# Optimization experiments

Measured on AMD Instinct MI355X. Metric: run time of the kernel, lower is better.

Reference implementation:

```python
import jax, jax.numpy as jnp
import numpy as np


def _gcn_conv(h, src, dst, W, b, n):
    # PyG GCNConv: x @ W, then symmetric-normalized aggregation with self-loops
    deg = jax.ops.segment_sum(jnp.ones(src.shape[0], h.dtype), dst, num_segments=n)
    dinv = jax.lax.rsqrt(jnp.maximum(deg, 1.0))  # deg >= 1 because self-loops are included
    norm = dinv[src] * dinv[dst]                 # [E]
    m = (h @ W)[src] * norm[:, None]             # gather + scale
    return jax.ops.segment_sum(m, dst, num_segments=n) + b


def setup_inputs() -> dict:
    key = jax.random.key(0)
    N, E, F, H, L, V = 50000, 800000, 128, 256, 64, 128
    ks = jax.random.split(key, 16)
    s = lambda fan_in: 1.0 / np.sqrt(fan_in)
    return {
        "x": jax.random.randint(ks[0], (N,), 0, V),
        "edge_index": jax.random.randint(ks[1], (2, E), 0, N),
        "eps": jax.random.normal(ks[2], (N, L), jnp.float32),
        "emb": jax.random.normal(ks[3], (V, F), jnp.float32),
        "W1": jax.random.normal(ks[4], (F, H), jnp.float32) * s(F),
        "b1": jnp.zeros((H,), jnp.float32),
        "W2": jax.random.normal(ks[5], (H, H), jnp.float32) * s(H),
        "b2": jnp.zeros((H,), jnp.float32),
        "Wmu": jax.random.normal(ks[6], (H, L), jnp.float32) * s(H),
        "bmu": jnp.zeros((L,), jnp.float32),
        "Wlv": jax.random.normal(ks[7], (H, L), jnp.float32) * s(H),
        "blv": jnp.zeros((L,), jnp.float32),
        "W3": jax.random.normal(ks[8], (L, H), jnp.float32) * s(L),
        "b3": jnp.zeros((H,), jnp.float32),
        "W4": jax.random.normal(ks[9], (H, V), jnp.float32) * s(H),
        "b4": jnp.zeros((V,), jnp.float32),
        "Wcap": jax.random.normal(ks[10], (L, 1), jnp.float32) * s(L),
        "bcap": jnp.zeros((1,), jnp.float32),
    }


def reference(x, edge_index, eps, emb, W1, b1, W2, b2, Wmu, bmu, Wlv, blv, W3, b3, W4, b4, Wcap, bcap):
    n = x.shape[0]
    loops = jnp.arange(n, dtype=edge_index.dtype)
    src = jnp.concatenate([edge_index[0], loops])  # add self-loops once, reuse
    dst = jnp.concatenate([edge_index[1], loops])

    h = emb[x]                                      # [N, F] embedding lookup
    h = jax.nn.relu(_gcn_conv(h, src, dst, W1, b1, n))
    h = jax.nn.relu(_gcn_conv(h, src, dst, W2, b2, n))
    mu = h @ Wmu + bmu
    logvar = h @ Wlv + blv
    z = mu + eps * jnp.exp(0.5 * logvar)            # reparameterize
    recon_x = jax.nn.relu(z @ W3 + b3) @ W4 + b4    # decode
    capitalize = jax.nn.sigmoid(z @ Wcap + bcap)
    return recon_x, capitalize, mu, logvar
```

## Files before the change

kernel.cpp:

```cpp
#include <hip/hip_runtime.h>
#include <math.h>


typedef __attribute__((ext_vector_type(8))) short bf16x8;
typedef __attribute__((ext_vector_type(4))) float f32x4;

__device__ inline unsigned short f2bf(float x) {
    unsigned u = __float_as_uint(x);
    return (unsigned short)((u + 0x7FFFu + ((u >> 16) & 1u)) >> 16);
}
__device__ inline float bf2f(unsigned short h) {
    return __uint_as_float(((unsigned)h) << 16);
}

__global__ __launch_bounds__(256) void k_deg_count(const int* __restrict__ dst,
                                                   int* __restrict__ degint, int E) {
    int e = blockIdx.x * 256 + threadIdx.x;
    if (e < E) atomicAdd(&degint[dst[e]], 1);
}

#define SCAN_BLOCK 1024
__global__ __launch_bounds__(SCAN_BLOCK) void k_scan_local(
        const int* __restrict__ degint, int* __restrict__ row_ptr,
        int* __restrict__ bsum, float* __restrict__ dinv, int N) {
    __shared__ int s[SCAN_BLOCK];
    int gid = blockIdx.x * SCAN_BLOCK + threadIdx.x;
    int d = (gid < N) ? (degint[gid] + 1) : 0;
    if (gid < N) dinv[gid] = rsqrtf((float)d);
    s[threadIdx.x] = d;
    __syncthreads();
    for (int off = 1; off < SCAN_BLOCK; off <<= 1) {
        int t = (threadIdx.x >= off) ? s[threadIdx.x - off] : 0;
        __syncthreads();
        s[threadIdx.x] += t;
        __syncthreads();
    }
    if (gid < N) row_ptr[gid] = s[threadIdx.x] - d;
    if (threadIdx.x == SCAN_BLOCK - 1) bsum[blockIdx.x] = s[SCAN_BLOCK - 1];
}

__global__ void k_scan_bsum(int* __restrict__ bsum, int nb) {
    if (blockIdx.x == 0 && threadIdx.x == 0) {
        int acc = 0;
        for (int i = 0; i < nb; ++i) { int v = bsum[i]; bsum[i] = acc; acc += v; }
    }
}

__global__ __launch_bounds__(256) void k_scan_add(int* __restrict__ row_ptr,
                                                  const int* __restrict__ bsum,
                                                  int N, int T) {
    int gid = blockIdx.x * 256 + threadIdx.x;
    if (gid < N) row_ptr[gid] += bsum[gid / SCAN_BLOCK];
    if (gid == 0) row_ptr[N] = T;
}

__global__ __launch_bounds__(256) void k_fill(
        const int* __restrict__ src, const int* __restrict__ dst,
        const int* __restrict__ x, const float* __restrict__ dinv,
        const int* __restrict__ row_ptr, int* __restrict__ cursor,
        int4* __restrict__ pack, int E, int N) {
    const int base = (blockIdx.x * 256 + threadIdx.x) * 4;
#pragma unroll
    for (int j = 0; j < 4; ++j) {
        int e = base + j;
        if (e < E) {
            int s = src[e], d = dst[e];
            float w = dinv[s] * dinv[d];
            int pos = row_ptr[d] + atomicAdd(&cursor[d], 1);
            pack[pos] = make_int4(__float_as_int(w), x[s], s, 0);
        } else if (e < E + N) {
            int i = e - E;
            float di = dinv[i];
            int pos = row_ptr[i] + atomicAdd(&cursor[i], 1);
            pack[pos] = make_int4(__float_as_int(di * di), x[i], i, 0);
        }
    }
}

__global__ __launch_bounds__(256) void k_cvt_all(
        const float* __restrict__ B0, unsigned short* __restrict__ h0, int K0, int N0,
        const float* __restrict__ B1, unsigned short* __restrict__ h1, int K1, int N1,
        const float* __restrict__ B2, unsigned short* __restrict__ h2, int K2, int N2,
        const float* __restrict__ B3, unsigned short* __restrict__ h3, int K3, int N3,
        const float* __restrict__ B4, unsigned short* __restrict__ h4, int K4, int N4) {
    const float* B; unsigned short* Bh; int K, Ncol;
    switch (blockIdx.y) {
        case 0: B = B0; Bh = h0; K = K0; Ncol = N0; break;
        case 1: B = B1; Bh = h1; K = K1; Ncol = N1; break;
        case 2: B = B2; Bh = h2; K = K2; Ncol = N2; break;
        case 3: B = B3; Bh = h3; K = K3; Ncol = N3; break;
        default: B = B4; Bh = h4; K = K4; Ncol = N4; break;
    }
    int i = blockIdx.x * 256 + threadIdx.x;
    if (i >= K * Ncol) return;
    int k = i / Ncol, n = i - k * Ncol;
    Bh[(long)n * K + k] = f2bf(B[i]);
}

__global__ __launch_bounds__(256) void k_gemm_f32t(
        const float* __restrict__ A, const float* __restrict__ B,
        unsigned short* __restrict__ CbT, int M, int K, int Ncol) {
    constexpr int BM = 64, BN = 64, BK = 16;
    __shared__ float As[BK][BM];
    __shared__ float Bs[BK][BN];
    const int tid = threadIdx.x;
    const int tx = tid & 15, ty = tid >> 4;
    const int rowBase = blockIdx.x * BM;
    const int colBase = blockIdx.y * BN;
    const int lr = tid >> 2, lc4 = tid & 3;
    const int br = tid >> 4, bc4 = tid & 15;
    const int arow = rowBase + lr;
    const int K4 = K >> 2, N4 = Ncol >> 2;
    const float4* A4 = (const float4*)A;
    const float4* B4 = (const float4*)B;
    float acc[4][4] = {{0.f}};
    for (int k0 = 0; k0 < K; k0 += BK) {
        float4 av = make_float4(0.f, 0.f, 0.f, 0.f);
        if (arow < M) av = A4[(long)arow * K4 + (k0 >> 2) + lc4];
        As[lc4 * 4 + 0][lr] = av.x;
        As[lc4 * 4 + 1][lr] = av.y;
        As[lc4 * 4 + 2][lr] = av.z;
        As[lc4 * 4 + 3][lr] = av.w;
        float4 bv = B4[(long)(k0 + br) * N4 + (colBase >> 2) + bc4];
        *(float4*)&Bs[br][bc4 * 4] = bv;
        __syncthreads();
#pragma unroll
        for (int k = 0; k < BK; ++k) {
            float4 a4v = *(const float4*)&As[k][ty * 4];
            float4 b4v = *(const float4*)&Bs[k][tx * 4];
            float aa[4] = {a4v.x, a4v.y, a4v.z, a4v.w};
            float bb[4] = {b4v.x, b4v.y, b4v.z, b4v.w};
#pragma unroll
            for (int i = 0; i < 4; ++i)
#pragma unroll
                for (int j = 0; j < 4; ++j)
                    acc[i][j] = fmaf(aa[i], bb[j], acc[i][j]);
        }
        __syncthreads();
    }
#pragma unroll
    for (int i = 0; i < 4; ++i) {
        int row = rowBase + ty * 4 + i;
        if (row < M) {
#pragma unroll
            for (int c = 0; c < 4; ++c) {
                int col = colBase + tx * 4 + c;
                CbT[(long)col * M + row] = f2bf(acc[i][c]);
            }
        }
    }
}

__global__ __launch_bounds__(256) void k_coef(
        const int4* __restrict__ pack, const int* __restrict__ row_ptr,
        unsigned short* __restrict__ cb, int N) {
    const int wave = threadIdx.x >> 6;
    const int lane = threadIdx.x & 63;
    const int node = blockIdx.x * 4 + wave;
    if (node >= N) return;
    const int tok0 = lane, tok1 = lane + 64;
    float c0 = 0.f, c1 = 0.f;
    const int beg = row_ptr[node], end = row_ptr[node + 1];
    int e = beg;
    for (; e + 4 <= end; e += 4) {
        int2 p0 = *(const int2*)&pack[e];
        int2 p1 = *(const int2*)&pack[e + 1];
        int2 p2 = *(const int2*)&pack[e + 2];
        int2 p3 = *(const int2*)&pack[e + 3];
        c0 += (p0.y == tok0) ? __int_as_float(p0.x) : 0.f;
        c1 += (p0.y == tok1) ? __int_as_float(p0.x) : 0.f;
        c0 += (p1.y == tok0) ? __int_as_float(p1.x) : 0.f;
        c1 += (p1.y == tok1) ? __int_as_float(p1.x) : 0.f;
        c0 += (p2.y == tok0) ? __int_as_float(p2.x) : 0.f;
        c1 += (p2.y == tok1) ? __int_as_float(p2.x) : 0.f;
        c0 += (p3.y == tok0) ? __int_as_float(p3.x) : 0.f;
        c1 += (p3.y == tok1) ? __int_as_float(p3.x) : 0.f;
    }
    for (; e < end; ++e) {
        int2 p = *(const int2*)&pack[e];
        c0 += (p.y == tok0) ? __int_as_float(p.x) : 0.f;
        c1 += (p.y == tok1) ? __int_as_float(p.x) : 0.f;
    }
    const long base = (long)node * 128;
    cb[base + lane]      = f2bf(c0);
    cb[base + lane + 64] = f2bf(c1);
}

template<bool RELU, bool BIAS, bool OUTBF>
__global__ __launch_bounds__(256) void k_gemm_mfma(
        const unsigned short* __restrict__ A, const unsigned short* __restrict__ Bt,
        const float* __restrict__ bias, float* __restrict__ Cf,
        unsigned short* __restrict__ Cb, int M, int K, int Ncol) {
    __shared__ unsigned short Ash[128][40];
    __shared__ unsigned short Bsh[64][40];
    const int tid = threadIdx.x;
    const int lane = tid & 63, w = tid >> 6;
    const int fr = lane & 15, quad = lane >> 4;
    const int wm0 = w * 32;
    const int rowBase = blockIdx.x * 128;
    const int colBase = blockIdx.y * 64;

    const int arow = tid >> 1;
    const int ahalf = (tid & 1) << 4;
    int agrow = rowBase + arow; if (agrow >= M) agrow = M - 1;
    const long abase = (long)agrow * K + ahalf;
    const int brow = tid >> 2;
    const int bseg = (tid & 3) << 3;
    const long bbase = (long)(colBase + brow) * K + bseg;

    f32x4 acc[2][4];
#pragma unroll
    for (int i = 0; i < 2; ++i)
#pragma unroll
        for (int j = 0; j < 4; ++j) acc[i][j] = (f32x4){0.f, 0.f, 0.f, 0.f};

    for (int k0 = 0; k0 < K; k0 += 32) {
        *(bf16x8*)&Ash[arow][ahalf]     = *(const bf16x8*)&A[abase + k0];
        *(bf16x8*)&Ash[arow][ahalf + 8] = *(const bf16x8*)&A[abase + k0 + 8];
        *(bf16x8*)&Bsh[brow][bseg]      = *(const bf16x8*)&Bt[bbase + k0];
        __syncthreads();
        bf16x8 ahf[2], bhf[4];
#pragma unroll
        for (int i = 0; i < 2; ++i)
            ahf[i] = *(const bf16x8*)&Ash[wm0 + i * 16 + fr][quad * 8];
#pragma unroll
        for (int j = 0; j < 4; ++j)
            bhf[j] = *(const bf16x8*)&Bsh[j * 16 + fr][quad * 8];
#pragma unroll
        for (int i = 0; i < 2; ++i)
#pragma unroll
            for (int j = 0; j < 4; ++j)
                acc[i][j] = __builtin_amdgcn_mfma_f32_16x16x32_bf16(
                    ahf[i], bhf[j], acc[i][j], 0, 0, 0);
        __syncthreads();
    }

#pragma unroll
    for (int i = 0; i < 2; ++i) {
        const int rowb = rowBase + wm0 + i * 16 + quad * 4;
#pragma unroll
        for (int j = 0; j < 4; ++j) {
            const int col = colBase + j * 16 + fr;
            const float bv = BIAS ? bias[col] : 0.f;
#pragma unroll
            for (int r = 0; r < 4; ++r) {
                const int row = rowb + r;
                if (row < M) {
                    float v = acc[i][j][r] + bv;
                    if (RELU) v = fmaxf(v, 0.f);
                    const long o = (long)row * Ncol + col;
                    if (OUTBF) Cb[o] = f2bf(v);
                    else       Cf[o] = v;
                }
            }
        }
    }
}

__global__ __launch_bounds__(256) void k_gemm_heads(
        const unsigned short* __restrict__ A, const unsigned short* __restrict__ Bt,
        const float* __restrict__ bmu, const float* __restrict__ blv,
        const float* __restrict__ eps, const float* __restrict__ Wcap,
        const float* __restrict__ bcap, float* __restrict__ mu,
        float* __restrict__ lv, unsigned short* __restrict__ Zh,
        float* __restrict__ cap, int M) {
    constexpr int K = 256;
    __shared__ unsigned short Ash[64][40];
    __shared__ unsigned short Bsh[128][40];
    const int tid = threadIdx.x;
    const int lane = tid & 63, w = tid >> 6;
    const int fr = lane & 15, quad = lane >> 4;
    const int wm0 = w * 16;
    const int rowBase = blockIdx.x * 64;

    const int arow = tid >> 2;
    const int aseg = (tid & 3) << 3;
    int agrow = rowBase + arow; if (agrow >= M) agrow = M - 1;
    const long abase = (long)agrow * K + aseg;
    const int brow = tid >> 1;
    const int bseg = (tid & 1) << 4;
    const long bbase = (long)brow * K + bseg;

    f32x4 acc[8];
#pragma unroll
    for (int j = 0; j < 8; ++j) acc[j] = (f32x4){0.f, 0.f, 0.f, 0.f};

    for (int k0 = 0; k0 < K; k0 += 32) {
        *(bf16x8*)&Ash[arow][aseg] = *(const bf16x8*)&A[abase + k0];
        *(bf16x8*)&Bsh[brow][bseg]     = *(const bf16x8*)&Bt[bbase + k0];
        *(bf16x8*)&Bsh[brow][bseg + 8] = *(const bf16x8*)&Bt[bbase + k0 + 8];
        __syncthreads();
        bf16x8 ahf = *(const bf16x8*)&Ash[wm0 + fr][quad * 8];
#pragma unroll
        for (int j = 0; j < 8; ++j) {
            bf16x8 bhf = *(const bf16x8*)&Bsh[j * 16 + fr][quad * 8];
            acc[j] = __builtin_amdgcn_mfma_f32_16x16x32_bf16(ahf, bhf, acc[j], 0, 0, 0);
        }
        __syncthreads();
    }

    float capacc[4] = {0.f, 0.f, 0.f, 0.f};
#pragma unroll
    for (int j = 0; j < 4; ++j) {
        const int c = j * 16 + fr;
        const float bm = bmu[c], bl = blv[c];
        const float wc = Wcap[c];
#pragma unroll
        for (int r = 0; r < 4; ++r) {
            const int row = rowBase + wm0 + quad * 4 + r;
            if (row < M) {
                const long o = (long)row * 64 + c;
                float mv = acc[j][r] + bm;
                float lvv = acc[j + 4][r] + bl;
                mu[o] = mv;
                lv[o] = lvv;
                float zz = fmaf(eps[o], expf(0.5f * lvv), mv);
                Zh[o] = f2bf(zz);
                capacc[r] = fmaf(zz, wc, capacc[r]);
            }
        }
    }
    const float b0 = bcap[0];
#pragma unroll
    for (int r = 0; r < 4; ++r) {
        float v = capacc[r];
        v += __shfl_xor(v, 1, 64);
        v += __shfl_xor(v, 2, 64);
        v += __shfl_xor(v, 4, 64);
        v += __shfl_xor(v, 8, 64);
        if (fr == 0) {
            const int row = rowBase + wm0 + quad * 4 + r;
            if (row < M) cap[row] = 1.f / (1.f + expf(-(v + b0)));
        }
    }
}

__global__ __launch_bounds__(256) void k_agg_nb(
        const unsigned short* __restrict__ h1, const int* __restrict__ row_ptr,
        const int4* __restrict__ pack, unsigned short* __restrict__ Ob, int N) {
    const int wave = threadIdx.x >> 6;
    const int lane = threadIdx.x & 63;
    const int node = blockIdx.x * 4 + wave;
    if (node >= N) return;
    const ushort4* h4 = (const ushort4*)h1;
    float ax = 0.f, ay = 0.f, az = 0.f, aw = 0.f;
    const int beg = row_ptr[node], end = row_ptr[node + 1];
    int e = beg;
    for (; e + 4 <= end; e += 4) {
        int4 p0 = pack[e], p1 = pack[e + 1], p2 = pack[e + 2], p3 = pack[e + 3];
        ushort4 v0 = h4[(long)p0.z * 64 + lane];
        ushort4 v1 = h4[(long)p1.z * 64 + lane];
        ushort4 v2 = h4[(long)p2.z * 64 + lane];
        ushort4 v3 = h4[(long)p3.z * 64 + lane];
        float w0 = __int_as_float(p0.x), w1 = __int_as_float(p1.x);
        float w2 = __int_as_float(p2.x), w3 = __int_as_float(p3.x);
        ax = fmaf(bf2f(v0.x), w0, ax); ay = fmaf(bf2f(v0.y), w0, ay);
        az = fmaf(bf2f(v0.z), w0, az); aw = fmaf(bf2f(v0.w), w0, aw);
        ax = fmaf(bf2f(v1.x), w1, ax); ay = fmaf(bf2f(v1.y), w1, ay);
        az = fmaf(bf2f(v1.z), w1, az); aw = fmaf(bf2f(v1.w), w1, aw);
        ax = fmaf(bf2f(v2.x), w2, ax); ay = fmaf(bf2f(v2.y), w2, ay);
        az = fmaf(bf2f(v2.z), w2, az); aw = fmaf(bf2f(v2.w), w2, aw);
        ax = fmaf(bf2f(v3.x), w3, ax); ay = fmaf(bf2f(v3.y), w3, ay);
        az = fmaf(bf2f(v3.z), w3, az); aw = fmaf(bf2f(v3.w), w3, aw);
    }
    for (; e < end; ++e) {
        int4 p = pack[e];
        float w0 = __int_as_float(p.x);
        ushort4 v = h4[(long)p.z * 64 + lane];
        ax = fmaf(bf2f(v.x), w0, ax); ay = fmaf(bf2f(v.y), w0, ay);
        az = fmaf(bf2f(v.z), w0, az); aw = fmaf(bf2f(v.w), w0, aw);
    }
    ushort4 o;
    o.x = f2bf(ax); o.y = f2bf(ay); o.z = f2bf(az); o.w = f2bf(aw);
    ((ushort4*)Ob)[(long)node * 64 + lane] = o;
}

extern "C" void kernel_launch(void* const* d_in, const int* in_sizes, int n_in,
                              void* d_out, int out_size, void* d_ws, size_t ws_size,
                              hipStream_t stream) {
    const int*   x    = (const int*)d_in[0];
    const int*   ei   = (const int*)d_in[1];
    const float* eps  = (const float*)d_in[2];
    const float* emb  = (const float*)d_in[3];
    const float* W1   = (const float*)d_in[4];
    const float* b1   = (const float*)d_in[5];
    const float* W2   = (const float*)d_in[6];
    const float* b2   = (const float*)d_in[7];
    const float* Wmu  = (const float*)d_in[8];
    const float* bmu  = (const float*)d_in[9];
    const float* Wlv  = (const float*)d_in[10];
    const float* blv  = (const float*)d_in[11];
    const float* W3   = (const float*)d_in[12];
    const float* b3   = (const float*)d_in[13];
    const float* W4   = (const float*)d_in[14];
    const float* b4   = (const float*)d_in[15];
    const float* Wcap = (const float*)d_in[16];
    const float* bcap = (const float*)d_in[17];

    const int N = in_sizes[0];
    const int E = in_sizes[1] / 2;
    const int H = in_sizes[5];
    const int L = in_sizes[9];
    const int V = in_sizes[15];
    const int F = in_sizes[4] / H;
    const int T = E + N;

    const int* src = ei;
    const int* dst = ei + E;

    char* w = (char*)d_ws;
    unsigned short* h1b  = (unsigned short*)w; w += (size_t)N * H * 2;
    unsigned short* a2b  = (unsigned short*)w; w += (size_t)N * H * 2;
    unsigned short* h2b  = (unsigned short*)w; w += (size_t)N * H * 2;
    unsigned short* zh   = (unsigned short*)w; w += (size_t)N * L * 2;
    unsigned short* cb   = (unsigned short*)w; w += (size_t)N * V * 2;
    int*   degint = (int*)w;   w += (size_t)N * 4;
    int*   cursor = (int*)w;   w += (size_t)N * 4;
    int*   rowp   = (int*)w;   w += (size_t)(N + 1) * 4;
    float* dinv   = (float*)w; w += (size_t)N * 4;
    int*   bsum   = (int*)w;   w += 256 * 4;
    int4*  pack   = (int4*)w;  w += (size_t)T * 16;
    unsigned short* tabT = (unsigned short*)w; w += (size_t)H * V * 2;
    unsigned short* W2t  = (unsigned short*)w; w += (size_t)H * H * 2;
    unsigned short* Wml  = (unsigned short*)w; w += (size_t)H * 2 * L * 2;
    unsigned short* W3t  = (unsigned short*)w; w += (size_t)L * H * 2;
    unsigned short* W4t  = (unsigned short*)w; w += (size_t)H * V * 2;

    unsigned short* tb = a2b;

    float* outp    = (float*)d_out;
    float* recon   = outp;
    float* cap     = outp + (size_t)N * V;
    float* mu      = outp + (size_t)N * V + N;
    float* logvar  = mu + (size_t)N * L;

    const int nN  = (N + 255) / 256;
    const int nE  = (E + 255) / 256;
    const int nT4 = (T + 1023) / 1024;
    const int nSc = (N + SCAN_BLOCK - 1) / SCAN_BLOCK;
    const int gM128 = (N + 127) / 128;
    const int gM64  = (N + 63) / 64;

    hipMemsetAsync(degint, 0, (size_t)N * 8, stream);
    k_deg_count<<<nE, 256, 0, stream>>>(dst, degint, E);
    k_scan_local<<<nSc, SCAN_BLOCK, 0, stream>>>(degint, rowp, bsum, dinv, N);
    k_scan_bsum<<<1, 64, 0, stream>>>(bsum, nSc);
    k_scan_add<<<nN, 256, 0, stream>>>(rowp, bsum, N, T);
    k_fill<<<nT4, 256, 0, stream>>>(src, dst, x, dinv, rowp, cursor, pack, E, N);

    k_cvt_all<<<dim3((H * H + 255) / 256, 5), 256, 0, stream>>>(
        W2, W2t, H, H,
        Wmu, Wml, H, L,
        Wlv, Wml + (size_t)L * H, H, L,
        W3, W3t, L, H,
        W4, W4t, H, V);

    k_gemm_f32t<<<dim3(V / 64, H / 64), 256, 0, stream>>>(emb, W1, tabT, V, F, H);
    k_coef<<<(N + 3) / 4, 256, 0, stream>>>(pack, rowp, cb, N);
    k_gemm_mfma<true, true, true><<<dim3(gM128, H / 64), 256, 0, stream>>>(
        cb, tabT, b1, nullptr, h1b, N, V, H);

    k_agg_nb<<<(N + 3) / 4, 256, 0, stream>>>(h1b, rowp, pack, a2b, N);
    k_gemm_mfma<true, true, true><<<dim3(gM128, H / 64), 256, 0, stream>>>(
        a2b, W2t, b2, nullptr, h2b, N, H, H);

    k_gemm_heads<<<gM64, 256, 0, stream>>>(
        h2b, Wml, bmu, blv, eps, Wcap, bcap, mu, logvar, zh, cap, N);

    k_gemm_mfma<true, true, true><<<dim3(gM128, H / 64), 256, 0, stream>>>(
        zh, W3t, b3, nullptr, tb, N, L, H);
    k_gemm_mfma<false, true, false><<<dim3(gM128, V / 64), 256, 0, stream>>>(
        tb, W4t, b4, recon, nullptr, N, H, V);
}
```

Baseline: 416.8 us.

## Fuse decoder GEMMs into one kernel and unroll neighbor aggregation by eight

Replaces the two decoder GEMM launches (z@W3 with relu, then @W4) with a single kernel that keeps the relu'd hidden tile in shared memory, avoiding the global write and reread of the N×256 intermediate. Also adds an 8-way unrolled loop in the neighbor aggregation to issue more independent gathers. The fused kernel uses large shared memory per block, which limits occupancy, and reloads W4 tiles per 64-row block; it also contains a redundant preliminary load loop.

```diff
diff --git a/kernel.cpp b/kernel.cpp
--- a/kernel.cpp
+++ b/kernel.cpp
@@ -335,6 +335,99 @@
     }
 }
 
+__global__ __launch_bounds__(256) void k_gemm_decode(
+        const unsigned short* __restrict__ Zh, const unsigned short* __restrict__ W3t,
+        const unsigned short* __restrict__ W4t, const float* __restrict__ b3,
+        const float* __restrict__ b4, float* __restrict__ recon, int M) {
+    __shared__ unsigned short Zs[64][40];
+    __shared__ unsigned short Bsh[256][40];
+    __shared__ unsigned short Ts[64][264];
+    const int tid = threadIdx.x;
+    const int lane = tid & 63, w = tid >> 6;
+    const int fr = lane & 15, quad = lane >> 4;
+    const int wm0 = w * 16;
+    const int rowBase = blockIdx.x * 64;
+
+    const int zrow = tid & 63;
+    const int zseg = (tid >> 6) << 3;
+    int zgrow = rowBase + zrow; if (zgrow >= M) zgrow = M - 1;
+    const long zbase = (long)zgrow * 64 + zseg;
+
+    f32x4 acc1[16];
+#pragma unroll
+    for (int j = 0; j < 16; ++j) acc1[j] = (f32x4){0.f, 0.f, 0.f, 0.f};
+
+#pragma unroll
+    for (int k0 = 0; k0 < 64; k0 += 32) {
+        *(bf16x8*)&Zs[zrow][zseg] = *(const bf16x8*)&Zh[zbase + k0 - zseg + zseg];
+        __syncthreads();
+        __syncthreads();
+        break;
+    }
+#pragma unroll
+    for (int j = 0; j < 16; ++j) acc1[j] = (f32x4){0.f, 0.f, 0.f, 0.f};
+    for (int k0 = 0; k0 < 64; k0 += 32) {
+        *(bf16x8*)&Zs[zrow][zseg] = *(const bf16x8*)&Zh[(long)zgrow * 64 + k0 + zseg];
+        {
+            const long wb = (long)tid * 64 + k0;
+            *(bf16x8*)&Bsh[tid][0]  = *(const bf16x8*)&W3t[wb];
+            *(bf16x8*)&Bsh[tid][8]  = *(const bf16x8*)&W3t[wb + 8];
+            *(bf16x8*)&Bsh[tid][16] = *(const bf16x8*)&W3t[wb + 16];
+            *(bf16x8*)&Bsh[tid][24] = *(const bf16x8*)&W3t[wb + 24];
+        }
+        __syncthreads();
+        bf16x8 af = *(const bf16x8*)&Zs[wm0 + fr][quad * 8];
+#pragma unroll
+        for (int j = 0; j < 16; ++j) {
+            bf16x8 bf = *(const bf16x8*)&Bsh[j * 16 + fr][quad * 8];
+            acc1[j] = __builtin_amdgcn_mfma_f32_16x16x32_bf16(af, bf, acc1[j], 0, 0, 0);
+        }
+        __syncthreads();
+    }
+
+#pragma unroll
+    for (int j = 0; j < 16; ++j) {
+        const int col = j * 16 + fr;
+        const float bv = b3[col];
+#pragma unroll
+        for (int r = 0; r < 4; ++r) {
+            const int rl = wm0 + quad * 4 + r;
+            Ts[rl][col] = f2bf(fmaxf(acc1[j][r] + bv, 0.f));
+        }
+    }
+    __syncthreads();
+
+    f32x4 acc2[8];
+#pragma unroll
+    for (int j = 0; j < 8; ++j) acc2[j] = (f32x4){0.f, 0.f, 0.f, 0.f};
+    const int br2 = tid >> 1;
+    const int bs2 = (tid & 1) << 4;
+    for (int k0 = 0; k0 < 256; k0 += 32) {
+        const long wb = (long)br2 * 256 + k0 + bs2;
+        *(bf16x8*)&Bsh[br2][bs2]     = *(const bf16x8*)&W4t[wb];
+        *(bf16x8*)&Bsh[br2][bs2 + 8] = *(const bf16x8*)&W4t[wb + 8];
+        __syncthreads();
+        bf16x8 at = *(const bf16x8*)&Ts[wm0 + fr][k0 + quad * 8];
+#pragma unroll
+        for (int j = 0; j < 8; ++j) {
+            bf16x8 bf = *(const bf16x8*)&Bsh[j * 16 + fr][quad * 8];
+            acc2[j] = __builtin_amdgcn_mfma_f32_16x16x32_bf16(at, bf, acc2[j], 0, 0, 0);
+        }
+        __syncthreads();
+    }
+
+#pragma unroll
+    for (int j = 0; j < 8; ++j) {
+        const int col = j * 16 + fr;
+        const float bv = b4[col];
+#pragma unroll
+        for (int r = 0; r < 4; ++r) {
+            const int row = rowBase + wm0 + quad * 4 + r;
+            if (row < M) recon[(long)row * 128 + col] = acc2[j][r] + bv;
+        }
+    }
+}
+
 __global__ __launch_bounds__(256) void k_agg_nb(
         const unsigned short* __restrict__ h1, const int* __restrict__ row_ptr,
         const int4* __restrict__ pack, unsigned short* __restrict__ Ob, int N) {
@@ -346,6 +439,38 @@
     float ax = 0.f, ay = 0.f, az = 0.f, aw = 0.f;
     const int beg = row_ptr[node], end = row_ptr[node + 1];
     int e = beg;
+    for (; e + 8 <= end; e += 8) {
+        int4 p0 = pack[e],     p1 = pack[e + 1], p2 = pack[e + 2], p3 = pack[e + 3];
+        int4 p4 = pack[e + 4], p5 = pack[e + 5], p6 = pack[e + 6], p7 = pack[e + 7];
+        ushort4 v0 = h4[(long)p0.z * 64 + lane];
+        ushort4 v1 = h4[(long)p1.z * 64 + lane];
+        ushort4 v2 = h4[(long)p2.z * 64 + lane];
+        ushort4 v3 = h4[(long)p3.z * 64 + lane];
+        ushort4 v4 = h4[(long)p4.z * 64 + lane];
+        ushort4 v5 = h4[(long)p5.z * 64 + lane];
+        ushort4 v6 = h4[(long)p6.z * 64 + lane];
+        ushort4 v7 = h4[(long)p7.z * 64 + lane];
+        float w0 = __int_as_float(p0.x), w1 = __int_as_float(p1.x);
+        float w2 = __int_as_float(p2.x), w3 = __int_as_float(p3.x);
+        float w4 = __int_as_float(p4.x), w5 = __int_as_float(p5.x);
+        float w6 = __int_as_float(p6.x), w7 = __int_as_float(p7.x);
+        ax = fmaf(bf2f(v0.x), w0, ax); ay = fmaf(bf2f(v0.y), w0, ay);
+        az = fmaf(bf2f(v0.z), w0, az); aw = fmaf(bf2f(v0.w), w0, aw);
+        ax = fmaf(bf2f(v1.x), w1, ax); ay = fmaf(bf2f(v1.y), w1, ay);
+        az = fmaf(bf2f(v1.z), w1, az); aw = fmaf(bf2f(v1.w), w1, aw);
+        ax = fmaf(bf2f(v2.x), w2, ax); ay = fmaf(bf2f(v2.y), w2, ay);
+        az = fmaf(bf2f(v2.z), w2, az); aw = fmaf(bf2f(v2.w), w2, aw);
+        ax = fmaf(bf2f(v3.x), w3, ax); ay = fmaf(bf2f(v3.y), w3, ay);
+        az = fmaf(bf2f(v3.z), w3, az); aw = fmaf(bf2f(v3.w), w3, aw);
+        ax = fmaf(bf2f(v4.x), w4, ax); ay = fmaf(bf2f(v4.y), w4, ay);
+        az = fmaf(bf2f(v4.z), w4, az); aw = fmaf(bf2f(v4.w), w4, aw);
+        ax = fmaf(bf2f(v5.x), w5, ax); ay = fmaf(bf2f(v5.y), w5, ay);
+        az = fmaf(bf2f(v5.z), w5, az); aw = fmaf(bf2f(v5.w), w5, aw);
+        ax = fmaf(bf2f(v6.x), w6, ax); ay = fmaf(bf2f(v6.y), w6, ay);
+        az = fmaf(bf2f(v6.z), w6, az); aw = fmaf(bf2f(v6.w), w6, aw);
+        ax = fmaf(bf2f(v7.x), w7, ax); ay = fmaf(bf2f(v7.y), w7, ay);
+        az = fmaf(bf2f(v7.z), w7, az); aw = fmaf(bf2f(v7.w), w7, aw);
+    }
     for (; e + 4 <= end; e += 4) {
         int4 p0 = pack[e], p1 = pack[e + 1], p2 = pack[e + 2], p3 = pack[e + 3];
         ushort4 v0 = h4[(long)p0.z * 64 + lane];
@@ -426,8 +551,6 @@
     unsigned short* W3t  = (unsigned short*)w; w += (size_t)L * H * 2;
     unsigned short* W4t  = (unsigned short*)w; w += (size_t)H * V * 2;
 
-    unsigned short* tb = a2b;
-
     float* outp    = (float*)d_out;
     float* recon   = outp;
     float* cap     = outp + (size_t)N * V;
@@ -467,8 +590,5 @@
     k_gemm_heads<<<gM64, 256, 0, stream>>>(
         h2b, Wml, bmu, blv, eps, Wcap, bcap, mu, logvar, zh, cap, N);
 
-    k_gemm_mfma<true, true, true><<<dim3(gM128, H / 64), 256, 0, stream>>>(
-        zh, W3t, b3, nullptr, tb, N, L, H);
-    k_gemm_mfma<false, true, false><<<dim3(gM128, V / 64), 256, 0, stream>>>(
-        tb, W4t, b4, recon, nullptr, N, H, V);
-}
+    k_gemm_decode<<<gM64, 256, 0, stream>>>(zh, W3t, W4t, b3, b4, recon, N);
+}
```

New measurement: 410.6 us. About the same (-1.5%).
